# Kernel optimization log

Hardware: AMD Instinct MI355X
Metric: run time of the kernel (lower is better)

Reference implementation:

```python
import jax, jax.numpy as jnp
import numpy as np

ENC_VTH = 0.999      # ENCODER_REGULAR_VTH
CDECAY = 0.5         # NEURON_CDECAY
VDECAY = 0.75        # NEURON_VDECAY
VTH = 0.5            # NEURON_VTH
WIN = 0.5            # SPIKE_PSEUDO_GRAD_WINDOW
T = 5                # spike_ts

# --- pseudo-gradient spike functions ---
@jax.custom_vjp
def enc_spike(v):
    return (v > ENC_VTH).astype(v.dtype)
def _enc_fwd(v):
    return enc_spike(v), None
def _enc_bwd(_, g):
    return (g,)  # straight-through
enc_spike.defvjp(_enc_fwd, _enc_bwd)

@jax.custom_vjp
def rect_spike(v):
    return (v > VTH).astype(v.dtype)
def _rect_fwd(v):
    return rect_spike(v), v
def _rect_bwd(v, g):
    return (g * (jnp.abs(v - VTH) < WIN).astype(g.dtype),)
rect_spike.defvjp(_rect_fwd, _rect_bwd)


def setup_inputs() -> dict:
    key = jax.random.key(0)
    ks = jax.random.split(key, 8)
    B, obs_dim, en_pop, act_dim, de_pop = 8192, 128, 10, 8, 10
    H1, H2 = 256, 256
    N = obs_dim * en_pop           # 1280
    O = act_dim * de_pop           # 80
    obs = jax.random.normal(ks[0], (B, obs_dim), jnp.float32)
    # encoder mean: linspace over mean_range per population, std constant 0.15
    mean_row = jnp.linspace(-3.0, 3.0, en_pop, dtype=jnp.float32)
    enc_mean = jnp.broadcast_to(mean_row, (1, obs_dim, en_pop)).astype(jnp.float32)
    enc_std = jnp.full((1, obs_dim, en_pop), 0.15, jnp.float32)
    W1 = jax.random.normal(ks[1], (H1, N), jnp.float32) / np.sqrt(N)
    b1 = jnp.zeros((H1,), jnp.float32)
    W2 = jax.random.normal(ks[2], (H2, H1), jnp.float32) / np.sqrt(H1)
    b2 = jnp.zeros((H2,), jnp.float32)
    Wo = jax.random.normal(ks[3], (O, H2), jnp.float32) / np.sqrt(H2)
    bo = jnp.zeros((O,), jnp.float32)
    dec_w = jax.random.normal(ks[4], (act_dim, de_pop), jnp.float32) / np.sqrt(de_pop)
    dec_b = jnp.zeros((act_dim,), jnp.float32)
    log_std = jnp.full((act_dim,), -0.001, jnp.float32)
    return {"obs": obs, "enc_mean": enc_mean, "enc_std": enc_std,
            "W1": W1, "b1": b1, "W2": W2, "b2": b2, "Wo": Wo, "bo": bo,
            "dec_w": dec_w, "dec_b": dec_b, "log_std": log_std}


def reference(obs, enc_mean, enc_std, W1, b1, W2, b2, Wo, bo, dec_w, dec_b, log_std):
    B = obs.shape[0]
    # --- population encoder: gaussian receptive fields -> regular spike train ---
    pop_act = jnp.exp(-0.5 * (obs[:, :, None] - enc_mean) ** 2 / enc_std ** 2)
    pop_act = pop_act.reshape(B, -1)  # [B, obs_dim*en_pop]

    def enc_step(volt, _):
        volt = volt + pop_act
        s = enc_spike(volt)
        return volt - s * ENC_VTH, s
    _, spikes = jax.lax.scan(enc_step, jnp.zeros_like(pop_act), None, length=T)  # [T, B, N]

    # --- LIF neuron model ---
    def lif(x, W, b, c, v, s):
        c = c * CDECAY + x @ W.T + b
        v = v * VDECAY * (1.0 - s) + c
        s = rect_spike(v)
        return c, v, s

    H1, H2, O = W1.shape[0], W2.shape[0], Wo.shape[0]
    z = lambda n: jnp.zeros((B, n), dtype=obs.dtype)
    carry0 = ((z(H1), z(H1), z(H1)), (z(H2), z(H2), z(H2)), (z(O), z(O), z(O)), z(O))

    def snn_step(carry, x):
        (c1, v1, s1), (c2, v2, s2), (co, vo, so), acc = carry
        c1, v1, s1 = lif(x, W1, b1, c1, v1, s1)
        c2, v2, s2 = lif(s1, W2, b2, c2, v2, s2)
        co, vo, so = lif(s2, Wo, bo, co, vo, so)
        return ((c1, v1, s1), (c2, v2, s2), (co, vo, so), acc + so), None

    (_, _, _, acc), _ = jax.lax.scan(snn_step, carry0, spikes)
    out_pop_act = acc / T  # [B, act_dim*de_pop]

    # --- grouped Conv1d(kernel=de_pop, groups=act_dim) decoder + ELU ---
    act_dim, de_pop = dec_w.shape
    mu = jax.nn.elu(jnp.einsum('bap,ap->ba', out_pop_act.reshape(B, act_dim, de_pop), dec_w) + dec_b)
    std = jnp.exp(log_std)
    return mu, std
```

## Files before the change

### kernel.cpp

```cpp
#include <hip/hip_runtime.h>

typedef unsigned short u16;
typedef unsigned int   u32;
typedef unsigned long long u64;
typedef __attribute__((ext_vector_type(8))) short bf16x8;
typedef __attribute__((ext_vector_type(4))) float f32x4;

#define NOBS 128
#define NN   1280
#define NH   256
#define NO   80
#define TT   5
#define RR   16
#define NTHR 512
#define BP1  88
#define BP2  20

#define W1TOT   983040
#define W2S_OFF 983040
#define WOS_OFF 1179648
#define WS_TOTAL 1277952

#define PREP_BLOCKS 4992

#define VMW2()  asm volatile("s_waitcnt vmcnt(2)" ::: "memory")
#define VMW0()  asm volatile("s_waitcnt vmcnt(0)" ::: "memory")
#define FENCE() asm volatile("" ::: "memory")

__device__ __forceinline__ float bf2f(u16 u) {
  union { u32 i; float f; } x; x.i = ((u32)u) << 16; return x.f;
}
__device__ __forceinline__ u16 f2bf(float f) {
  union { float f; u32 i; } x; x.f = f;
  u32 i = x.i + 0x7FFFu + ((x.i >> 16) & 1u);
  return (u16)(i >> 16);
}

__device__ __forceinline__ u16 split3(float w, int sel) {
  u16 hi = f2bf(w);
  if (sel == 0) return hi;
  float r1 = __fsub_rn(w, bf2f(hi));
  u16 mid = f2bf(r1);
  if (sel == 1) return mid;
  float r2 = __fsub_rn(r1, bf2f(mid));
  return f2bf(r2);
}

__device__ __forceinline__ float exp_cr(float arg) {
  double xa = (double)arg;
  double nd = __builtin_rint(xa * 1.4426950408889634074);
  double r  = fma(nd, -6.93147180369123816490e-01, xa);
  r         = fma(nd, -1.90821492927058770002e-10, r);
  double p = 2.50521083854417187751e-08;
  p = fma(p, r, 2.75573192239858906526e-07);
  p = fma(p, r, 2.75573192239858906526e-06);
  p = fma(p, r, 2.48015873015873015873e-05);
  p = fma(p, r, 1.98412698412698412698e-04);
  p = fma(p, r, 1.38888888888888888889e-03);
  p = fma(p, r, 8.33333333333333333333e-03);
  p = fma(p, r, 4.16666666666666666667e-02);
  p = fma(p, r, 1.66666666666666666667e-01);
  p = fma(p, r, 0.5);
  p = fma(p, r, 1.0);
  p = fma(p, r, 1.0);
  int n = (int)nd;
  union { u64 u; double d; } s;
  s.u = ((u64)(u32)(n + 1023)) << 52;
  return (n < -150) ? 0.f : (float)(s.d * p);
}

__global__ __launch_bounds__(256) void prep_w(
    const float* __restrict__ W1, const float* __restrict__ W2,
    const float* __restrict__ Wo, u16* __restrict__ ws)
{
  int i = blockIdx.x * 256 + threadIdx.x;
  if (i < W1TOT) {
    int kc = i / 49152, r = i - kc * 49152;
    int ks = r / 24576, r2 = r - ks * 24576;
    int sel = r2 / 8192, r3 = r2 & 8191;
    int j = r3 >> 5, kkpos = r3 & 31;
    int kk = ((kkpos >> 3) ^ ((j >> 1) & 3)) * 8 + (kkpos & 7);
    ws[i] = split3(W1[j * 1280 + kc * 64 + ks * 32 + kk], sel);
  } else if (i < WOS_OFF) {
    int i2 = i - W2S_OFF;
    int kc = i2 / 49152, r = i2 - kc * 49152;
    int ks = r / 24576, r2 = r - ks * 24576;
    int sel = r2 / 8192, r3 = r2 & 8191;
    int j = r3 >> 5, kkpos = r3 & 31;
    int kk = ((kkpos >> 3) ^ ((j >> 1) & 3)) * 8 + (kkpos & 7);
    ws[i] = split3(W2[j * 256 + kc * 64 + ks * 32 + kk], sel);
  } else {
    int i3 = i - WOS_OFF;
    int kc = i3 / 24576, r = i3 - kc * 24576;
    int ks = r / 12288, r2 = r - ks * 12288;
    int sel = r2 / 4096, r3 = r2 & 4095;
    int j = r3 >> 5, kkpos = r3 & 31;
    int kk = ((kkpos >> 3) ^ ((j >> 1) & 3)) * 8 + (kkpos & 7);
    float w = (j < NO) ? Wo[j * 256 + kc * 64 + ks * 32 + kk] : 0.f;
    ws[i] = split3(w, sel);
  }
}

__device__ __forceinline__ void dma2(const u16* __restrict__ src, u16* dst, int lane) {
  __builtin_amdgcn_global_load_lds((const u32*)(src + lane * 8), (u32*)dst, 16, 0, 0);
  __builtin_amdgcn_global_load_lds((const u32*)(src + 512 + lane * 8),
                                   (u32*)(dst + 512), 16, 0, 0);
}

__device__ __forceinline__ void gemm_wp(
    const u16* lbits, int bpitch,
    const u16* __restrict__ wsbase, int nkc, int selblk,
    u16* mybuf,
    int wv, int lane, f32x4 acc[2][TT])
{
  const int m16 = lane & 15, q = lane >> 4;
  const int swz = (q ^ ((m16 >> 1) & 3)) * 8;
  const int lro0 = m16 * 32 + swz;
  const int lro1 = lro0 + 512;
  const int sh = q * 8;
  const int nst = nkc * 6;
  const u16* slice = wsbase + wv * 1024;

  dma2(slice, mybuf, lane);
  dma2(slice + selblk, mybuf + 1024, lane);
  FENCE();

  int st = 0;
  for (int kcks = 0; kcks < nkc * 2; ++kcks) {
    const int kc = kcks >> 1, ks = kcks & 1;
    bf16x8 afr[TT];
    #pragma unroll
    for (int t = 0; t < TT; ++t) {
      u32 bwv = *(const u32*)(lbits + (t * RR + m16) * bpitch + kc * 4 + ks * 2);
      u32 b = (bwv >> sh) & 0xFFu;
      union { u32 u[4]; bf16x8 v; } x;
      #pragma unroll
      for (int i = 0; i < 4; ++i)
        x.u[i] = ((((b >> (2 * i)) & 3u) * 0x8001u) & 0x00010001u) * 0x3F80u;
      afr[t] = x.v;
    }
    #pragma unroll
    for (int sel = 0; sel < 3; ++sel, ++st) {
      u16* cur = mybuf + sel * 1024;
      if (st + 1 < nst) { VMW2(); } else { VMW0(); }
      const bf16x8 bf0 = *(const bf16x8*)(cur + lro0);
      const bf16x8 bf1 = *(const bf16x8*)(cur + lro1);
      #pragma unroll
      for (int t = 0; t < TT; ++t)
        acc[0][t] = __builtin_amdgcn_mfma_f32_16x16x32_bf16(afr[t], bf0, acc[0][t], 0, 0, 0);
      #pragma unroll
      for (int t = 0; t < TT; ++t)
        acc[1][t] = __builtin_amdgcn_mfma_f32_16x16x32_bf16(afr[t], bf1, acc[1][t], 0, 0, 0);
      FENCE();
      if (st + 2 < nst)
        dma2(slice + (st + 2) * selblk, mybuf + ((sel + 2) % 3) * 1024, lane);
      FENCE();
    }
  }
}

__device__ __forceinline__ void recur_spikes2(
    f32x4 acc[2][TT], const float* __restrict__ bias,
    int lane, int wv, u16* sbits, int spitch)
{
  const int q = lane >> 4, m16 = lane & 15;
  #pragma unroll
  for (int i = 0; i < 2; ++i) {
    int ct = wv * 2 + i;
    int j = ct * 16 + m16;
    float bj = bias[j];
    #pragma unroll
    for (int rg = 0; rg < 4; ++rg) {
      float c = 0.f, v = 0.f, sprev = 0.f;
      #pragma unroll
      for (int t = 0; t < TT; ++t) {
        float u = acc[i][t][rg];
        c = __fadd_rn(__fadd_rn(__fmul_rn(c, 0.5f), u), bj);
        float vd = __fmul_rn(v, 0.75f);
        v = __fadd_rn((sprev > 0.5f) ? 0.f : vd, c);
        bool sp = v > 0.5f;
        u64 mask = __ballot(sp);
        if (m16 == 0) {
          int row = q * 4 + rg;
          sbits[(t * RR + row) * spitch + ct] = (u16)(mask >> (q * 16));
        }
        sprev = sp ? 1.f : 0.f;
      }
    }
  }
}

__global__ __launch_bounds__(NTHR, 4) void snn_main(
    const float* __restrict__ obs, const float* __restrict__ enc_mean,
    const float* __restrict__ enc_std,
    const float* __restrict__ b1, const float* __restrict__ b2, const float* __restrict__ bo,
    const float* __restrict__ dec_w, const float* __restrict__ dec_b, const float* __restrict__ log_std,
    const u16* __restrict__ wsW, float* __restrict__ out, int Btot)
{
  __shared__ __align__(16) u16 smem[37376];
  u16* bufs = smem;
  u16* encb = smem + 24576;
  u16* s1b  = encb + 7040;
  u16* s2b  = s1b + 1600;
  float* soacc = (float*)(s2b + 1600);

  const int tid  = threadIdx.x;
  const int lane = tid & 63;
  const int wv   = tid >> 6;
  const int r0   = blockIdx.x * RR;
  u16* mybuf = bufs + wv * 3072;

  for (int it = tid; it < RR * 80; it += NTHR) {
    int r = it / 80, w = it - (it / 80) * 80;
    const float* obsrow = obs + (r0 + r) * NOBS;
    u32 wbits[TT] = {0, 0, 0, 0, 0};
    #pragma unroll 4
    for (int e = 0; e < 16; ++e) {
      int k = w * 16 + e;
      int f = k / 10;
      float x  = obsrow[f];
      float m  = enc_mean[k];
      float sd = enc_std[k];
      float d  = __fsub_rn(x, m);
      float arg = __fdiv_rn(__fmul_rn(-0.5f, __fmul_rn(d, d)), __fmul_rn(sd, sd));
      float a = exp_cr(arg);
      float v = 0.f;
      #pragma unroll
      for (int t = 0; t < TT; ++t) {
        v = __fadd_rn(v, a);
        if (v > 0.999f) { wbits[t] |= (1u << e); v = __fsub_rn(v, 0.999f); }
      }
    }
    #pragma unroll
    for (int t = 0; t < TT; ++t)
      encb[(t * RR + r) * BP1 + w] = (u16)wbits[t];
  }
  __syncthreads();

  f32x4 acc[2][TT];
  const f32x4 zero4 = {0.f, 0.f, 0.f, 0.f};
#define ZERO_ACC() { _Pragma("unroll") for (int i = 0; i < 2; ++i) \
                     _Pragma("unroll") for (int t = 0; t < TT; ++t) acc[i][t] = zero4; }

  ZERO_ACC();
  gemm_wp(encb, BP1, wsW, 20, 8192, mybuf, wv, lane, acc);
  recur_spikes2(acc, b1, lane, wv, s1b, BP2);
  __syncthreads();

  ZERO_ACC();
  gemm_wp(s1b, BP2, wsW + W2S_OFF, 4, 8192, mybuf, wv, lane, acc);
  recur_spikes2(acc, b2, lane, wv, s2b, BP2);
  __syncthreads();

  if (wv < 3) {
    ZERO_ACC();
    gemm_wp(s2b, BP2, wsW + WOS_OFF, 4, 4096, mybuf, wv, lane, acc);
    const int q = lane >> 4, m16 = lane & 15;
    #pragma unroll
    for (int i = 0; i < 2; ++i) {
      int j = (wv * 2 + i) * 16 + m16;
      bool valid = j < NO;
      float bj = valid ? bo[j] : 0.f;
      #pragma unroll
      for (int rg = 0; rg < 4; ++rg) {
        float c = 0.f, v = 0.f, sprev = 0.f;
        int cnt = 0;
        #pragma unroll
        for (int t = 0; t < TT; ++t) {
          float u = acc[i][t][rg];
          c = __fadd_rn(__fadd_rn(__fmul_rn(c, 0.5f), u), bj);
          float vd = __fmul_rn(v, 0.75f);
          v = __fadd_rn((sprev > 0.5f) ? 0.f : vd, c);
          bool sp = v > 0.5f;
          cnt += sp ? 1 : 0;
          sprev = sp ? 1.f : 0.f;
        }
        if (valid) soacc[(q * 4 + rg) * NO + j] = __fdiv_rn((float)cnt, 5.0f);
      }
    }
  }
  __syncthreads();

  if (tid < RR * 8) {
    int r = tid >> 3, a = tid & 7;
    float s = 0.f;
    const float* so = soacc + r * NO + a * 10;
    #pragma unroll
    for (int p = 0; p < 10; ++p)
      s = __fadd_rn(s, __fmul_rn(so[p], dec_w[a * 10 + p]));
    s = __fadd_rn(s, dec_b[a]);
    float mu = (s > 0.f) ? s : expm1f(s);
    out[(r0 + r) * 8 + a] = mu;
  }
  if (blockIdx.x == 0 && tid < 8) {
    out[Btot * 8 + tid] = expf(log_std[tid]);
  }
}

extern "C" void kernel_launch(void* const* d_in, const int* in_sizes, int n_in,
                              void* d_out, int out_size, void* d_ws, size_t ws_size,
                              hipStream_t stream) {
  const float* obs      = (const float*)d_in[0];
  const float* enc_mean = (const float*)d_in[1];
  const float* enc_std  = (const float*)d_in[2];
  const float* W1       = (const float*)d_in[3];
  const float* b1       = (const float*)d_in[4];
  const float* W2       = (const float*)d_in[5];
  const float* b2       = (const float*)d_in[6];
  const float* Wo       = (const float*)d_in[7];
  const float* bo       = (const float*)d_in[8];
  const float* dec_w    = (const float*)d_in[9];
  const float* dec_b    = (const float*)d_in[10];
  const float* log_std  = (const float*)d_in[11];
  u16*   ws  = (u16*)d_ws;
  float* out = (float*)d_out;
  int B = in_sizes[0] / NOBS;

  hipLaunchKernelGGL(prep_w, dim3(PREP_BLOCKS), dim3(256), 0, stream,
                     W1, W2, Wo, ws);
  hipLaunchKernelGGL(snn_main, dim3(B / RR), dim3(NTHR), 0, stream,
                     obs, enc_mean, enc_std, b1, b2, bo, dec_w, dec_b, log_std,
                     ws, out, B);
}
```

Measured before the change: 182.5 us.

## Prefetch next LDS weight fragment during MFMAs and halve encoder work per thread

The GEMM loop now issues the next DMA first, runs the MFMAs on fragments already held in registers, and only then waits and reads the following buffer's fragments from LDS. This overlaps LDS reads with MFMA execution instead of stalling before each MFMA group. Separately, the encoder loop gives each thread 8 neurons instead of 16, writing bytes instead of 16-bit words, so 2560 work items spread over 512 threads and the loop load balances better. The register-held fragments raise register pressure, and byte-granular LDS stores add store instructions.

```diff
diff --git a/kernel.cpp b/kernel.cpp
--- a/kernel.cpp
+++ b/kernel.cpp
@@ -1,5 +1,6 @@
 #include <hip/hip_runtime.h>
 
+typedef unsigned char  u8;
 typedef unsigned short u16;
 typedef unsigned int   u32;
 typedef unsigned long long u64;
@@ -124,6 +125,10 @@
   dma2(slice, mybuf, lane);
   dma2(slice + selblk, mybuf + 1024, lane);
   FENCE();
+  VMW2();
+  bf16x8 cur0 = *(const bf16x8*)(mybuf + lro0);
+  bf16x8 cur1 = *(const bf16x8*)(mybuf + lro1);
+  FENCE();
 
   int st = 0;
   for (int kcks = 0; kcks < nkc * 2; ++kcks) {
@@ -141,19 +146,21 @@
     }
     #pragma unroll
     for (int sel = 0; sel < 3; ++sel, ++st) {
-      u16* cur = mybuf + sel * 1024;
-      if (st + 1 < nst) { VMW2(); } else { VMW0(); }
-      const bf16x8 bf0 = *(const bf16x8*)(cur + lro0);
-      const bf16x8 bf1 = *(const bf16x8*)(cur + lro1);
-      #pragma unroll
-      for (int t = 0; t < TT; ++t)
-        acc[0][t] = __builtin_amdgcn_mfma_f32_16x16x32_bf16(afr[t], bf0, acc[0][t], 0, 0, 0);
-      #pragma unroll
-      for (int t = 0; t < TT; ++t)
-        acc[1][t] = __builtin_amdgcn_mfma_f32_16x16x32_bf16(afr[t], bf1, acc[1][t], 0, 0, 0);
-      FENCE();
       if (st + 2 < nst)
         dma2(slice + (st + 2) * selblk, mybuf + ((sel + 2) % 3) * 1024, lane);
+      FENCE();
+      #pragma unroll
+      for (int t = 0; t < TT; ++t)
+        acc[0][t] = __builtin_amdgcn_mfma_f32_16x16x32_bf16(afr[t], cur0, acc[0][t], 0, 0, 0);
+      #pragma unroll
+      for (int t = 0; t < TT; ++t)
+        acc[1][t] = __builtin_amdgcn_mfma_f32_16x16x32_bf16(afr[t], cur1, acc[1][t], 0, 0, 0);
+      if (st + 1 < nst) {
+        if (st + 2 < nst) { VMW2(); } else { VMW0(); }
+        const u16* nb = mybuf + ((sel + 1) % 3) * 1024;
+        cur0 = *(const bf16x8*)(nb + lro0);
+        cur1 = *(const bf16x8*)(nb + lro1);
+      }
       FENCE();
     }
   }
@@ -210,13 +217,14 @@
   const int r0   = blockIdx.x * RR;
   u16* mybuf = bufs + wv * 3072;
 
-  for (int it = tid; it < RR * 80; it += NTHR) {
-    int r = it / 80, w = it - (it / 80) * 80;
+  for (int h = tid; h < RR * 160; h += NTHR) {
+    int r = h / 160, rem = h - r * 160;
+    int w = rem >> 1, hi = rem & 1;
     const float* obsrow = obs + (r0 + r) * NOBS;
-    u32 wbits[TT] = {0, 0, 0, 0, 0};
-    #pragma unroll 4
-    for (int e = 0; e < 16; ++e) {
-      int k = w * 16 + e;
+    u32 bits[TT] = {0, 0, 0, 0, 0};
+    #pragma unroll
+    for (int e = 0; e < 8; ++e) {
+      int k = w * 16 + hi * 8 + e;
       int f = k / 10;
       float x  = obsrow[f];
       float m  = enc_mean[k];
@@ -228,12 +236,13 @@
       #pragma unroll
       for (int t = 0; t < TT; ++t) {
         v = __fadd_rn(v, a);
-        if (v > 0.999f) { wbits[t] |= (1u << e); v = __fsub_rn(v, 0.999f); }
+        if (v > 0.999f) { bits[t] |= (1u << e); v = __fsub_rn(v, 0.999f); }
       }
     }
+    u8* eb = (u8*)encb;
     #pragma unroll
     for (int t = 0; t < TT; ++t)
-      encb[(t * RR + r) * BP1 + w] = (u16)wbits[t];
+      eb[((t * RR + r) * BP1 + w) * 2 + hi] = (u8)bits[t];
   }
   __syncthreads();
 
```

After: 178.0 us. 2.5% less time.
